# Performance work log

Measured on AMD Instinct MI355X. Metric: run time of the kernel, lower is better.

## Reference

```python
import jax, jax.numpy as jnp
import numpy as np

# Structural metadata (constants): 3 node types, 4 edge types, 2 HGT layers.
T, R, L = 3, 4, 2
H_HID, HEADS, OUT = 256, 8, 128
D = H_HID // HEADS  # per-head dim = 32
SRC_T = (0, 1, 1, 1)  # (author->paper, paper->author, paper->paper, paper->venue)
DST_T = (1, 0, 1, 2)
LN_EPS = 1e-5


def _segment_softmax(logits, seg, n):
    # logits: [E, heads]; softmax over edges sharing the same destination node
    m = jax.ops.segment_max(logits, seg, num_segments=n)
    e = jnp.exp(logits - m[seg])
    s = jax.ops.segment_sum(e, seg, num_segments=n)
    return e / s[seg]


def setup_inputs() -> dict:
    key = jax.random.key(0)
    ks = iter(jax.random.split(key, 64))
    N, E, FIN = 20000, 60000, 128

    def nrm(shape, scale):
        return jax.random.normal(next(ks), shape, jnp.float32) * scale

    return dict(
        x=jax.random.normal(next(ks), (T, N, FIN), jnp.float32),
        edge_index=jax.random.randint(next(ks), (R, 2, E), 0, N),
        Win=nrm((T, FIN, H_HID), 0.05),
        b_in=jnp.zeros((T, H_HID), jnp.float32),
        Wk=nrm((L, T, H_HID, H_HID), 0.05), bk=jnp.zeros((L, T, H_HID), jnp.float32),
        Wq=nrm((L, T, H_HID, H_HID), 0.05), bq=jnp.zeros((L, T, H_HID), jnp.float32),
        Wv=nrm((L, T, H_HID, H_HID), 0.05), bv=jnp.zeros((L, T, H_HID), jnp.float32),
        Wa=nrm((L, T, H_HID, H_HID), 0.05), ba=jnp.zeros((L, T, H_HID), jnp.float32),
        skip=jnp.ones((L, T), jnp.float32),
        a_rel=nrm((L, R, HEADS, D, D), 0.1),
        m_rel=nrm((L, R, HEADS, D, D), 0.1),
        p_rel=jnp.ones((L, R, HEADS), jnp.float32),
        ln_g=jnp.ones((L, T, H_HID), jnp.float32),
        ln_b=jnp.zeros((L, T, H_HID), jnp.float32),
        Wout=nrm((H_HID, OUT), 0.05),
        bout=jnp.zeros((OUT,), jnp.float32),
    )


def reference(x, edge_index, Win, b_in, Wk, bk, Wq, bq, Wv, bv, Wa, ba,
              skip, a_rel, m_rel, p_rel, ln_g, ln_b, Wout, bout):
    N = x.shape[1]
    inv_sqrt_d = jnp.float32(1.0 / np.sqrt(D))
    # Input projection + ReLU (dropout = identity in eval mode)
    h = jax.nn.relu(jnp.einsum('tnf,tfh->tnh', x, Win) + b_in[:, None, :])

    for l in range(L):
        res = h
        # Per-node-type k/q/v projections, reshaped to heads
        k = (jnp.einsum('tnh,tho->tno', h, Wk[l]) + bk[l][:, None]).reshape(T, N, HEADS, D)
        q = (jnp.einsum('tnh,tho->tno', h, Wq[l]) + bq[l][:, None]).reshape(T, N, HEADS, D)
        v = (jnp.einsum('tnh,tho->tno', h, Wv[l]) + bv[l][:, None]).reshape(T, N, HEADS, D)

        agg = jnp.zeros((T, N, HEADS, D), h.dtype)
        for r in range(R):
            st, dt = SRC_T[r], DST_T[r]
            src, dst = edge_index[r, 0], edge_index[r, 1]
            # Per-edge-type relation transforms on source k/v
            k_r = jnp.einsum('nhd,hde->nhe', k[st], a_rel[l, r])
            v_r = jnp.einsum('nhd,hde->nhe', v[st], m_rel[l, r])
            kj = k_r[src]          # [E, heads, d]
            vj = v_r[src]
            qi = q[dt][dst]
            logits = (qi * kj).sum(-1) * p_rel[l, r] * inv_sqrt_d  # [E, heads]
            alpha = _segment_softmax(logits, dst, N)
            msg = vj * alpha[..., None]
            agg = agg.at[dt].add(jax.ops.segment_sum(msg, dst, num_segments=N))

        # Type-specific output linear after exact GELU, gated skip (in==out dims)
        o = jax.nn.gelu(agg.reshape(T, N, H_HID), approximate=False)
        o = jnp.einsum('tnh,tho->tno', o, Wa[l]) + ba[l][:, None]
        beta = jax.nn.sigmoid(skip[l])[:, None, None]
        h = beta * o + (1.0 - beta) * h

        # Model-level residual + LayerNorm + ReLU (dropout = identity)
        h = h + res
        mu = h.mean(-1, keepdims=True)
        var = ((h - mu) ** 2).mean(-1, keepdims=True)
        h = (h - mu) * jax.lax.rsqrt(var + LN_EPS) * ln_g[l][:, None] + ln_b[l][:, None]
        h = jax.nn.relu(h)

    # Shared output projection; outputs stacked over node types: [T, N, OUT]
    return jnp.einsum('tnh,ho->tno', h, Wout) + bout
```

## Files before the change

### kernel.cpp

```cpp
#include <hip/hip_runtime.h>
#include <math.h>

#define T_ 3
#define R_ 4
#define L_ 2
#define H_ 256
#define HEADS_ 8
#define D_ 32
#define FIN_ 128
#define OUT_ 128

typedef unsigned short bf16_t;
typedef __attribute__((ext_vector_type(8))) short bf16x8;
typedef __attribute__((ext_vector_type(4))) float f32x4;

__device__ __forceinline__ float bf2f(bf16_t h) {
    return __uint_as_float(((unsigned)h) << 16);
}
__device__ __forceinline__ float bflo(unsigned u) {
    return __uint_as_float(u << 16);
}
__device__ __forceinline__ float bfhi(unsigned u) {
    return __uint_as_float(u & 0xffff0000u);
}
__device__ __forceinline__ bf16_t f2bf(float f) {
    unsigned u = __float_as_uint(f);
    u += 0x7FFFu + ((u >> 16) & 1u);
    return (bf16_t)(u >> 16);
}
__device__ __forceinline__ float gelu_exact(float x) {
    return 0.5f * x * (1.0f + erff(x * 0.70710678118654752440f));
}

__global__ void zero_kernel(unsigned* __restrict__ p, long n) {
    long i = (long)blockIdx.x * blockDim.x + threadIdx.x;
    long stride = (long)gridDim.x * blockDim.x;
    for (; i < n; i += stride) p[i] = 0u;
}

__global__ __launch_bounds__(256) void transconv2_kernel(
    const float* __restrict__ in0, bf16_t* __restrict__ out0,
    const float* __restrict__ in1, bf16_t* __restrict__ out1,
    int cnt0, int Rr, int Cc)
{
    __shared__ float Ls[64][65];
    const int tid = threadIdx.x;
    int z = blockIdx.z;
    const float* in;
    bf16_t* out;
    if (z < cnt0) { in = in0; out = out0; }
    else          { in = in1; out = out1; z -= cnt0; }
    const long base = (long)z * Rr * Cc;
    const int r0 = blockIdx.y * 64, c0 = blockIdx.x * 64;
    #pragma unroll
    for (int i = 0; i < 16; ++i) {
        int e = tid + i * 256; int row = e >> 6, col = e & 63;
        Ls[row][col] = in[base + (long)(r0 + row) * Cc + c0 + col];
    }
    __syncthreads();
    #pragma unroll
    for (int i = 0; i < 16; ++i) {
        int e = tid + i * 256; int row = e >> 6, col = e & 63;
        out[base + (long)(c0 + row) * Rr + r0 + col] = f2bf(Ls[col][row]);
    }
}

__global__ __launch_bounds__(256) void transconv_kernel(
    const float* __restrict__ in, bf16_t* __restrict__ out, int Rr, int Cc)
{
    __shared__ float Ls[64][65];
    const int tid = threadIdx.x;
    const long base = (long)blockIdx.z * Rr * Cc;
    const int r0 = blockIdx.y * 64, c0 = blockIdx.x * 64;
    #pragma unroll
    for (int i = 0; i < 16; ++i) {
        int e = tid + i * 256; int row = e >> 6, col = e & 63;
        Ls[row][col] = in[base + (long)(r0 + row) * Cc + c0 + col];
    }
    __syncthreads();
    #pragma unroll
    for (int i = 0; i < 16; ++i) {
        int e = tid + i * 256; int row = e >> 6, col = e & 63;
        out[base + (long)(c0 + row) * Rr + r0 + col] = f2bf(Ls[col][row]);
    }
}

__global__ __launch_bounds__(256) void fuse_wT_kernel(
    const float* __restrict__ Wk, const float* __restrict__ Wv,
    const float* __restrict__ bk, const float* __restrict__ bv,
    const float* __restrict__ a_rel, const float* __restrict__ m_rel,
    bf16_t* __restrict__ WkvT, float* __restrict__ bkv)
{
    const int s = blockIdx.z;
    const int kv = s & 1, r = (s >> 1) & 3, l = s >> 3;
    const int SRCT[4] = {0, 1, 1, 1};
    const int st = SRCT[r];
    const float* W = (kv ? Wv : Wk) + ((long)l * T_ + st) * H_ * H_;
    const float* A = (kv ? m_rel : a_rel) + ((long)l * R_ + r) * HEADS_ * D_ * D_;
    const int hh = blockIdx.y, kt = blockIdx.x;
    __shared__ float As[32][33];
    __shared__ float Ws[64][33];
    const int tid = threadIdx.x;
    {
        int d = tid >> 3, e4 = (tid & 7) * 4;
        float4 v = *(const float4*)(A + (hh * D_ + d) * D_ + e4);
        As[d][e4] = v.x; As[d][e4 + 1] = v.y; As[d][e4 + 2] = v.z; As[d][e4 + 3] = v.w;
    }
    #pragma unroll
    for (int p = 0; p < 2; ++p) {
        int idx = p * 256 + tid;
        int row = idx >> 3, c4 = (idx & 7) * 4;
        float4 v = *(const float4*)(W + (long)(kt * 64 + row) * H_ + hh * 32 + c4);
        Ws[row][c4] = v.x; Ws[row][c4 + 1] = v.y; Ws[row][c4 + 2] = v.z; Ws[row][c4 + 3] = v.w;
    }
    __syncthreads();
    const int kl = tid & 63, eb = tid >> 6;
    #pragma unroll
    for (int ii = 0; ii < 8; ++ii) {
        int e = eb * 8 + ii;
        float acc = 0.f;
        #pragma unroll
        for (int d = 0; d < 32; ++d)
            acc += As[d][e] * Ws[kl][d];
        int col = hh * 32 + e;
        int pos = (col >> 2) * 8 + kv * 4 + (col & 3);
        long rowIdx = (long)(s >> 1) * 512 + pos;
        WkvT[rowIdx * H_ + kt * 64 + kl] = f2bf(acc);
    }
    if (blockIdx.x == 0 && blockIdx.y == 0) {
        const float* b = (kv ? bv : bk) + ((long)l * T_ + st) * H_;
        const int bh = tid >> 5, be = tid & 31;
        float acc = 0.f;
        #pragma unroll
        for (int d = 0; d < D_; ++d)
            acc += b[bh * D_ + d] * A[(bh * D_ + d) * D_ + be];
        int pos = (tid >> 2) * 8 + kv * 4 + (tid & 3);
        bkv[(long)(s >> 1) * 512 + pos] = acc;
    }
}

__global__ void hist_kernel(const int* __restrict__ ei, int* __restrict__ indeg,
                            int Nn, int E)
{
    int idx = blockIdx.x * 256 + threadIdx.x;
    if (idx >= R_ * E) return;
    int r = idx / E, e = idx - r * E;
    int d = ei[(size_t)r * 2 * E + E + e];
    atomicAdd(indeg + (size_t)r * Nn + d, 1);
}

__global__ __launch_bounds__(256) void csr_part_kernel(
    const int* __restrict__ indeg, int* __restrict__ partials, int Nn, int nch)
{
    const int r = blockIdx.y, c = blockIdx.x, tid = threadIdx.x;
    const int lane = tid & 63, wave = tid >> 6;
    int idx = c * 256 + tid;
    int v = (idx < Nn) ? indeg[(size_t)r * Nn + idx] : 0;
    #pragma unroll
    for (int off = 1; off < 64; off <<= 1) v += __shfl_xor(v, off);
    __shared__ int wsum[4];
    if (lane == 0) wsum[wave] = v;
    __syncthreads();
    if (tid == 0) partials[r * nch + c] = wsum[0] + wsum[1] + wsum[2] + wsum[3];
}

__global__ __launch_bounds__(256) void csr_scanpart_kernel(
    int* __restrict__ partials, int nch)
{
    const int r = blockIdx.x, tid = threadIdx.x;
    __shared__ int sh[256];
    int v = (tid < nch) ? partials[r * nch + tid] : 0;
    sh[tid] = v;
    __syncthreads();
    for (int off = 1; off < 256; off <<= 1) {
        int u = (tid >= off) ? sh[tid - off] : 0;
        __syncthreads();
        sh[tid] += u;
        __syncthreads();
    }
    if (tid < nch) partials[r * nch + tid] = sh[tid] - v;
}

__global__ __launch_bounds__(256) void csr_write_kernel(
    const int* __restrict__ indeg, const int* __restrict__ partials,
    int* __restrict__ offs, int* __restrict__ cursor, int Nn, int nch)
{
    const int r = blockIdx.y, c = blockIdx.x, tid = threadIdx.x;
    int idx = c * 256 + tid;
    int v = (idx < Nn) ? indeg[(size_t)r * Nn + idx] : 0;
    __shared__ int sh[256];
    sh[tid] = v;
    __syncthreads();
    for (int off = 1; off < 256; off <<= 1) {
        int u = (tid >= off) ? sh[tid - off] : 0;
        __syncthreads();
        sh[tid] += u;
        __syncthreads();
    }
    int incl = sh[tid];
    int base = partials[r * nch + c];
    if (idx < Nn) {
        int excl = base + incl - v;
        offs[(size_t)r * (Nn + 1) + idx] = excl;
        cursor[(size_t)r * Nn + idx] = excl;
        if (idx == Nn - 1) offs[(size_t)r * (Nn + 1) + Nn] = base + incl;
    }
}

__global__ void scatter_kernel(const int* __restrict__ ei, int* __restrict__ cursor,
                               int* __restrict__ esrc, int Nn, int E)
{
    int idx = blockIdx.x * 256 + threadIdx.x;
    if (idx >= R_ * E) return;
    int r = idx / E, e = idx - r * E;
    int s = ei[(size_t)r * 2 * E + e];
    int d = ei[(size_t)r * 2 * E + E + e];
    int pos = atomicAdd(cursor + (size_t)r * Nn + d, 1);
    esrc[(size_t)r * E + pos] = s * 512;
}

#define STEP(rr, vld, prX, mX, sX, x0, x1, x2, x3)                          \
    {                                                                        \
        float dt_ = q0 * bflo(rr.x) + q1 * bfhi(rr.x)                        \
                  + q2 * bflo(rr.y) + q3 * bfhi(rr.y);                       \
        dt_ += __shfl_xor(dt_, 1);                                           \
        dt_ += __shfl_xor(dt_, 2);                                           \
        dt_ += __shfl_xor(dt_, 4);                                           \
        float lg = (vld) ? dt_ * prX : -1e30f;                               \
        if (__any(lg - mX > 8.f)) {                                          \
            float mn = fmaxf(mX, lg);                                        \
            float fac = __expf(mX - mn);                                     \
            float p = __expf(lg - mn);                                       \
            p = (vld) ? p : 0.f;                                             \
            sX = sX * fac + p;                                               \
            x0 = x0 * fac + p * bflo(rr.z);                                  \
            x1 = x1 * fac + p * bfhi(rr.z);                                  \
            x2 = x2 * fac + p * bflo(rr.w);                                  \
            x3 = x3 * fac + p * bfhi(rr.w);                                  \
            mX = mn;                                                         \
        } else {                                                             \
            float p = __expf(lg - mX);                                       \
            p = (vld) ? p : 0.f;                                             \
            sX += p;                                                         \
            x0 += p * bflo(rr.z);                                            \
            x1 += p * bfhi(rr.z);                                            \
            x2 += p * bflo(rr.w);                                            \
            x3 += p * bfhi(rr.w);                                            \
        }                                                                    \
    }

__global__ __launch_bounds__(256) void agg_all_kernel(
    const int* __restrict__ offs, const int* __restrict__ esrc,
    bf16_t* __restrict__ qbuf, const bf16_t* __restrict__ KV,
    const float* __restrict__ p_l, float scale, int Nn, int E)
{
    static const int NRELg[3] = {2, 1, 1};
    static const int R0g[3]  = {0, 1, 3};
    static const int R1g[3]  = {2, 0, 0};
    static const int DTg[3]  = {1, 0, 2};
    const int grp = blockIdx.y;
    const int wave = threadIdx.x >> 6, lane = threadIdx.x & 63;
    const int d = blockIdx.x * 4 + wave;
    if (d >= Nn) return;
    const int head = lane >> 3;
    const int dt = DTg[grp];
    const bool separate = (NRELg[grp] == 2);

    bf16_t* qrow = qbuf + ((size_t)dt * Nn + d) * H_;
    uint2 qu = ((const uint2*)qrow)[lane];
    float q0 = bflo(qu.x), q1 = bfhi(qu.x), q2 = bflo(qu.y), q3 = bfhi(qu.y);

    const int rA = R0g[grp];
    const int* esA = esrc + (size_t)rA * E;
    const bf16_t* kvA = KV + (size_t)rA * Nn * 512;
    float prA = p_l[rA * HEADS_ + head] * scale;
    int curA = offs[(size_t)rA * (Nn + 1) + d];
    int endA = offs[(size_t)rA * (Nn + 1) + d + 1];

    const int* esB; const bf16_t* kvB; float prB;
    int curB, endB;
    if (separate) {
        const int rB = R1g[grp];
        esB = esrc + (size_t)rB * E;
        kvB = KV + (size_t)rB * Nn * 512;
        prB = p_l[rB * HEADS_ + head] * scale;
        curB = offs[(size_t)rB * (Nn + 1) + d];
        endB = offs[(size_t)rB * (Nn + 1) + d + 1];
    } else {
        int mid = curA + ((endA - curA + 1) >> 1);
        esB = esA; kvB = kvA; prB = prA;
        curB = mid; endB = endA;
        endA = mid;
    }
    const int safeA = (endA > 0) ? endA - 1 : 0;
    const int safeB = (endB > 0) ? endB - 1 : 0;
    const int loff = lane * 8;

    float mA = -INFINITY, sA = 0.f, aA0 = 0.f, aA1 = 0.f, aA2 = 0.f, aA3 = 0.f;
    float mB = -INFINITY, sB = 0.f, aB0 = 0.f, aB1 = 0.f, aB2 = 0.f, aB3 = 0.f;

    while (curA < endA || curB < endB) {
        bool vA0 = curA < endA, vA1 = curA + 1 < endA;
        bool vB0 = curB < endB, vB1 = curB + 1 < endB;
        uint4 rA0, rA1, rB0, rB1;
        if (vA0) {
            int i0 = esA[curA];
            int i1 = esA[min(curA + 1, safeA)];
            rA0 = *(const uint4*)(kvA + i0 + loff);
            rA1 = *(const uint4*)(kvA + i1 + loff);
        }
        if (vB0) {
            int i0 = esB[curB];
            int i1 = esB[min(curB + 1, safeB)];
            rB0 = *(const uint4*)(kvB + i0 + loff);
            rB1 = *(const uint4*)(kvB + i1 + loff);
        }
        if (vA0) {
            STEP(rA0, true, prA, mA, sA, aA0, aA1, aA2, aA3)
            STEP(rA1, vA1, prA, mA, sA, aA0, aA1, aA2, aA3)
            curA += 2;
        }
        if (vB0) {
            STEP(rB0, true, prB, mB, sB, aB0, aB1, aB2, aB3)
            STEP(rB1, vB1, prB, mB, sB, aB0, aB1, aB2, aB3)
            curB += 2;
        }
    }

    float t0, t1, t2, t3;
    if (separate) {
        float iA = (sA > 0.f) ? 1.f / sA : 0.f;
        float iB = (sB > 0.f) ? 1.f / sB : 0.f;
        t0 = aA0 * iA + aB0 * iB;
        t1 = aA1 * iA + aB1 * iB;
        t2 = aA2 * iA + aB2 * iB;
        t3 = aA3 * iA + aB3 * iB;
    } else {
        if (sB > 0.f) {
            float mm = fmaxf(mA, mB);
            float fx = (sA > 0.f) ? __expf(mA - mm) : 0.f;
            float fy = __expf(mB - mm);
            sA = sA * fx + sB * fy;
            aA0 = aA0 * fx + aB0 * fy;
            aA1 = aA1 * fx + aB1 * fy;
            aA2 = aA2 * fx + aB2 * fy;
            aA3 = aA3 * fx + aB3 * fy;
        }
        float iA = (sA > 0.f) ? 1.f / sA : 0.f;
        t0 = aA0 * iA; t1 = aA1 * iA; t2 = aA2 * iA; t3 = aA3 * iA;
    }
    ushort4 ou;
    ou.x = f2bf(gelu_exact(t0));
    ou.y = f2bf(gelu_exact(t1));
    ou.z = f2bf(gelu_exact(t2));
    ou.w = f2bf(gelu_exact(t3));
    ((ushort4*)qrow)[lane] = ou;
}

#define ASTR 40
#define ESTR 72

template<typename TA, typename TC, int ACT_C>
__global__ __launch_bounds__(256) void mfma_gemm(
    const TA* __restrict__ A, const TA* __restrict__ A2, int zsplit,
    const bf16_t* __restrict__ BT,
    const float* __restrict__ bias, TC* __restrict__ C,
    int M, int K, int Nc,
    long strideA, long strideB, long strideBias, long strideC)
{
    const int gX = gridDim.x, gY = gridDim.y, gZ = gridDim.z;
    const int nwg = gX * gY * gZ;
    int flat = blockIdx.x + gX * (blockIdx.y + gY * blockIdx.z);
    const int qch = nwg >> 3, rch = nwg & 7;
    int xcd = flat & 7, cidx = flat >> 3;
    int swz = (xcd < rch ? xcd * (qch + 1) : rch * (qch + 1) + (xcd - rch) * qch) + cidx;
    const int by = swz / (gX * gZ);
    int rem = swz - by * (gX * gZ);
    const int bz = rem / gX;
    const int bx = rem - bz * gX;

    const TA* Ab = (bz < zsplit) ? (A + (long)bz * strideA) : A2;
    const bf16_t* Bb = BT + (long)bz * strideB;
    const float* biasb = bias + (long)bz * strideBias;
    TC* Cb = C + (long)bz * strideC;

    __shared__ bf16_t As[128 * ASTR];
    __shared__ bf16_t Bs[128 * ASTR];
    __shared__ bf16_t Es[4 * 16 * ESTR];
    const int tid = threadIdx.x;
    const int lane = tid & 63, wave = tid >> 6;
    const int wr = wave >> 1, wc = wave & 1;
    const int bm = by * 128, bn = bx * 128;
    const int r16 = lane & 15, g = lane >> 4;
    f32x4 acc[4][4] = {};

    for (int k0 = 0; k0 < K; k0 += 32) {
        #pragma unroll
        for (int p = 0; p < 2; ++p) {
            int idx = p * 256 + tid;
            int row = idx >> 2, seg = idx & 3;
            int grow = bm + row;
            bf16x8 av = {};
            if (grow < M) {
                if constexpr (sizeof(TA) == 2) {
                    av = *(const bf16x8*)(Ab + (long)grow * K + k0 + seg * 8);
                } else {
                    const float* sp = (const float*)Ab + (long)grow * K + k0 + seg * 8;
                    float4 f0 = *(const float4*)sp, f1 = *(const float4*)(sp + 4);
                    av[0] = (short)f2bf(f0.x); av[1] = (short)f2bf(f0.y);
                    av[2] = (short)f2bf(f0.z); av[3] = (short)f2bf(f0.w);
                    av[4] = (short)f2bf(f1.x); av[5] = (short)f2bf(f1.y);
                    av[6] = (short)f2bf(f1.z); av[7] = (short)f2bf(f1.w);
                }
            }
            *(bf16x8*)(As + row * ASTR + seg * 8) = av;
            bf16x8 bv = *(const bf16x8*)(Bb + (long)(bn + row) * K + k0 + seg * 8);
            *(bf16x8*)(Bs + row * ASTR + seg * 8) = bv;
        }
        __syncthreads();
        bf16x8 af[4], bfr[4];
        #pragma unroll
        for (int m = 0; m < 4; ++m)
            af[m] = *(const bf16x8*)(As + (wr * 64 + m * 16 + r16) * ASTR + g * 8);
        #pragma unroll
        for (int n = 0; n < 4; ++n)
            bfr[n] = *(const bf16x8*)(Bs + (wc * 64 + n * 16 + r16) * ASTR + g * 8);
        #pragma unroll
        for (int m = 0; m < 4; ++m)
            #pragma unroll
            for (int n = 0; n < 4; ++n)
                acc[m][n] = __builtin_amdgcn_mfma_f32_16x16x32_bf16(af[m], bfr[n], acc[m][n], 0, 0, 0);
        __syncthreads();
    }

    float bb[4];
    #pragma unroll
    for (int n = 0; n < 4; ++n)
        bb[n] = biasb[bn + wc * 64 + n * 16 + r16];

    if constexpr (sizeof(TC) == 2) {
        bf16_t* st = Es + wave * (16 * ESTR);
        #pragma unroll
        for (int m = 0; m < 4; ++m) {
            int rowbase = bm + wr * 64 + m * 16;
            #pragma unroll
            for (int n = 0; n < 4; ++n) {
                #pragma unroll
                for (int j = 0; j < 4; ++j) {
                    float vv = acc[m][n][j] + bb[n];
                    if (ACT_C) vv = fmaxf(vv, 0.f);
                    st[(g * 4 + j) * ESTR + n * 16 + r16] = f2bf(vv);
                }
            }
            #pragma unroll
            for (int p = 0; p < 2; ++p) {
                int row = p * 8 + (lane >> 3);
                int col0 = (lane & 7) * 8;
                int grow = rowbase + row;
                bf16x8 val = *(const bf16x8*)(st + row * ESTR + col0);
                if (grow < M)
                    *(bf16x8*)(Cb + (long)grow * Nc + bn + wc * 64 + col0) = val;
            }
        }
    } else {
        #pragma unroll
        for (int n = 0; n < 4; ++n) {
            int col = bn + wc * 64 + n * 16 + r16;
            #pragma unroll
            for (int m = 0; m < 4; ++m) {
                int rowbase = bm + wr * 64 + m * 16 + g * 4;
                #pragma unroll
                for (int j = 0; j < 4; ++j) {
                    int row = rowbase + j;
                    if (row < M) {
                        float vv = acc[m][n][j] + bb[n];
                        if (ACT_C) vv = fmaxf(vv, 0.f);
                        Cb[(long)row * Nc + col] = vv;
                    }
                }
            }
        }
    }
}

__global__ __launch_bounds__(512) void gemm_ln_kernel(
    const bf16_t* __restrict__ A,
    const bf16_t* __restrict__ BT,
    const float* __restrict__ bias,
    bf16_t* __restrict__ h,
    const float* __restrict__ skip_l,
    const float* __restrict__ ln_g,
    const float* __restrict__ ln_b,
    int M)
{
    const int gY = gridDim.y;
    const int nwg = gY * 3;
    int flat = blockIdx.y + gY * blockIdx.z;
    const int qch = nwg >> 3, rch = nwg & 7;
    int xcd = flat & 7, cidx = flat >> 3;
    int swz = (xcd < rch ? xcd * (qch + 1) : rch * (qch + 1) + (xcd - rch) * qch) + cidx;
    const int by = swz / 3;
    const int bz = swz - by * 3;

    const bf16_t* Ab = A + (long)bz * M * H_;
    const bf16_t* Bb = BT + (long)bz * H_ * H_;
    const float* biasb = bias + bz * H_;
    bf16_t* hb = h + (long)bz * M * H_;
    const float* lgp = ln_g + bz * H_;
    const float* lbp = ln_b + bz * H_;

    __shared__ bf16_t As[128 * ASTR];
    __shared__ bf16_t Bs[256 * ASTR];
    __shared__ bf16_t Es[8 * 16 * ESTR];
    __shared__ float  sums[128][4][2];

    const int tid = threadIdx.x;
    const int lane = tid & 63, wave = tid >> 6;
    const int wr = wave >> 2, wc = wave & 3;
    const int bm = by * 128;
    const int r16 = lane & 15, g = lane >> 4;
    f32x4 acc[4][4] = {};

    for (int k0 = 0; k0 < H_; k0 += 32) {
        {
            int row = tid >> 2, seg = tid & 3;
            int grow = bm + row;
            bf16x8 av = {};
            if (grow < M) av = *(const bf16x8*)(Ab + (long)grow * H_ + k0 + seg * 8);
            *(bf16x8*)(As + row * ASTR + seg * 8) = av;
        }
        #pragma unroll
        for (int p = 0; p < 2; ++p) {
            int idx = p * 512 + tid;
            int row = idx >> 2, seg = idx & 3;
            bf16x8 bv = *(const bf16x8*)(Bb + (long)row * H_ + k0 + seg * 8);
            *(bf16x8*)(Bs + row * ASTR + seg * 8) = bv;
        }
        __syncthreads();
        bf16x8 af[4], bfr[4];
        #pragma unroll
        for (int m = 0; m < 4; ++m)
            af[m] = *(const bf16x8*)(As + (wr * 64 + m * 16 + r16) * ASTR + g * 8);
        #pragma unroll
        for (int n = 0; n < 4; ++n)
            bfr[n] = *(const bf16x8*)(Bs + (wc * 64 + n * 16 + r16) * ASTR + g * 8);
        #pragma unroll
        for (int m = 0; m < 4; ++m)
            #pragma unroll
            for (int n = 0; n < 4; ++n)
                acc[m][n] = __builtin_amdgcn_mfma_f32_16x16x32_bf16(af[m], bfr[n], acc[m][n], 0, 0, 0);
        __syncthreads();
    }

    const float beta = 1.f / (1.f + __expf(-skip_l[bz]));
    const float cb = 2.f - beta;
    const int colb = wc * 64;
    float bb[4], lng[4], lnb[4];
    #pragma unroll
    for (int n = 0; n < 4; ++n) {
        int col = colb + n * 16 + r16;
        bb[n] = biasb[col]; lng[n] = lgp[col]; lnb[n] = lbp[col];
    }

    bf16_t* st = Es + wave * (16 * ESTR);
    #pragma unroll
    for (int m = 0; m < 4; ++m) {
        #pragma unroll
        for (int p = 0; p < 2; ++p) {
            int row = p * 8 + (lane >> 3);
            int col0 = (lane & 7) * 8;
            int grow = bm + wr * 64 + m * 16 + row;
            bf16x8 hv = {};
            if (grow < M) hv = *(const bf16x8*)(hb + (long)grow * H_ + colb + col0);
            *(bf16x8*)(st + row * ESTR + col0) = hv;
        }
        #pragma unroll
        for (int j = 0; j < 4; ++j) {
            int lrow = wr * 64 + m * 16 + g * 4 + j;
            float s1 = 0.f, s2 = 0.f;
            #pragma unroll
            for (int n = 0; n < 4; ++n) {
                float o = acc[m][n][j] + bb[n];
                float hv = bf2f(st[(g * 4 + j) * ESTR + n * 16 + r16]);
                float u = beta * o + cb * hv;
                acc[m][n][j] = u;
                s1 += u; s2 += u * u;
            }
            s1 += __shfl_xor(s1, 1); s2 += __shfl_xor(s2, 1);
            s1 += __shfl_xor(s1, 2); s2 += __shfl_xor(s2, 2);
            s1 += __shfl_xor(s1, 4); s2 += __shfl_xor(s2, 4);
            s1 += __shfl_xor(s1, 8); s2 += __shfl_xor(s2, 8);
            if (r16 == 0) { sums[lrow][wc][0] = s1; sums[lrow][wc][1] = s2; }
        }
    }
    __syncthreads();

    #pragma unroll
    for (int m = 0; m < 4; ++m) {
        #pragma unroll
        for (int j = 0; j < 4; ++j) {
            int lrow = wr * 64 + m * 16 + g * 4 + j;
            float S1 = sums[lrow][0][0] + sums[lrow][1][0] + sums[lrow][2][0] + sums[lrow][3][0];
            float S2 = sums[lrow][0][1] + sums[lrow][1][1] + sums[lrow][2][1] + sums[lrow][3][1];
            float mu = S1 * (1.f / H_);
            float var = S2 * (1.f / H_) - mu * mu;
            float inv = rsqrtf(var + 1e-5f);
            #pragma unroll
            for (int n = 0; n < 4; ++n) {
                float r = fmaxf((acc[m][n][j] - mu) * inv * lng[n] + lnb[n], 0.f);
                st[(g * 4 + j) * ESTR + n * 16 + r16] = f2bf(r);
            }
        }
        #pragma unroll
        for (int p = 0; p < 2; ++p) {
            int row = p * 8 + (lane >> 3);
            int col0 = (lane & 7) * 8;
            int grow = bm + wr * 64 + m * 16 + row;
            bf16x8 val = *(const bf16x8*)(st + row * ESTR + col0);
            if (grow < M)
                *(bf16x8*)(hb + (long)grow * H_ + colb + col0) = val;
        }
    }
}

extern "C" void kernel_launch(void* const* d_in, const int* in_sizes, int n_in,
                              void* d_out, int out_size, void* d_ws, size_t ws_size,
                              hipStream_t stream)
{
    const float* x     = (const float*)d_in[0];
    const int*   ei    = (const int*)  d_in[1];
    const float* Win   = (const float*)d_in[2];
    const float* b_in  = (const float*)d_in[3];
    const float* Wk    = (const float*)d_in[4];
    const float* bk    = (const float*)d_in[5];
    const float* Wq    = (const float*)d_in[6];
    const float* bq    = (const float*)d_in[7];
    const float* Wv    = (const float*)d_in[8];
    const float* bv    = (const float*)d_in[9];
    const float* Wa    = (const float*)d_in[10];
    const float* ba    = (const float*)d_in[11];
    const float* skip  = (const float*)d_in[12];
    const float* a_rel = (const float*)d_in[13];
    const float* m_rel = (const float*)d_in[14];
    const float* p_rel = (const float*)d_in[15];
    const float* ln_g  = (const float*)d_in[16];
    const float* ln_b  = (const float*)d_in[17];
    const float* Wout  = (const float*)d_in[18];
    const float* bout  = (const float*)d_in[19];
    float* out = (float*)d_out;

    const int N = in_sizes[0] / (T_ * FIN_);
    const int E = in_sizes[1] / (R_ * 2);
    const size_t NH = (size_t)N * H_;
    const int nch = (N + 255) / 256;
    const int ZBIG = 1 << 20;

    char* wp = (char*)d_ws;
    auto alloc = [&](size_t bytes) {
        void* r = wp;
        wp += (bytes + 255) & ~(size_t)255;
        return r;
    };
    bf16_t* h     = (bf16_t*)alloc(T_ * NH * 2);
    bf16_t* qbuf  = (bf16_t*)alloc(T_ * NH * 2);
    bf16_t* KV    = (bf16_t*)alloc((size_t)R_ * N * 512 * 2);
    int*    indeg = (int*)   alloc((size_t)R_ * N * 4);
    int*    offs  = (int*)   alloc((size_t)R_ * (N + 1) * 4);
    int*    cursor= (int*)   alloc((size_t)R_ * N * 4);
    int*    esrc  = (int*)   alloc((size_t)R_ * E * 4);
    int*    parts = (int*)   alloc((size_t)R_ * 256 * 4);
    bf16_t* WqT   = (bf16_t*)alloc((size_t)L_ * T_ * H_ * H_ * 2);
    bf16_t* WaT   = (bf16_t*)alloc((size_t)L_ * T_ * H_ * H_ * 2);
    bf16_t* WinT  = (bf16_t*)alloc((size_t)T_ * FIN_ * H_ * 2);
    bf16_t* WoutT = (bf16_t*)alloc((size_t)H_ * OUT_ * 2);
    bf16_t* WkvT  = (bf16_t*)alloc((size_t)L_ * R_ * 512 * H_ * 2);
    float*  bkv   = (float*) alloc((size_t)L_ * R_ * 512 * 4);

    if ((size_t)(wp - (char*)d_ws) > ws_size) return;

    const float scale = 0.17677669529663688f;
    dim3 blk(256);
    auto gM = [](long M) { return (int)((M + 127) / 128); };

    transconv2_kernel<<<dim3(4, 4, 2 * L_ * T_), blk, 0, stream>>>(
        Wq, WqT, Wa, WaT, L_ * T_, H_, H_);
    transconv_kernel<<<dim3(4, 2, T_), blk, 0, stream>>>(Win, WinT, FIN_, H_);
    transconv_kernel<<<dim3(2, 4, 1),  blk, 0, stream>>>(Wout, WoutT, H_, OUT_);
    fuse_wT_kernel<<<dim3(4, 8, 16), blk, 0, stream>>>(
        Wk, Wv, bk, bv, a_rel, m_rel, WkvT, bkv);

    zero_kernel<<<256, blk, 0, stream>>>((unsigned*)indeg, (long)R_ * N);
    hist_kernel<<<(R_ * E + 255) / 256, blk, 0, stream>>>(ei, indeg, N, E);
    csr_part_kernel<<<dim3(nch, R_), blk, 0, stream>>>(indeg, parts, N, nch);
    csr_scanpart_kernel<<<R_, blk, 0, stream>>>(parts, nch);
    csr_write_kernel<<<dim3(nch, R_), blk, 0, stream>>>(indeg, parts, offs, cursor, N, nch);
    scatter_kernel<<<(R_ * E + 255) / 256, blk, 0, stream>>>(ei, cursor, esrc, N, E);

    mfma_gemm<float, bf16_t, 1><<<dim3(H_ / 128, gM(N), T_), blk, 0, stream>>>(
        x, x, ZBIG, WinT, b_in, h, N, FIN_, H_,
        (long)N * FIN_, (long)FIN_ * H_, H_, (long)NH);

    for (int l = 0; l < L_; ++l) {
        const long lw = (long)l * R_;
        mfma_gemm<bf16_t, bf16_t, 0><<<dim3(512 / 128, gM(N), 4), blk, 0, stream>>>(
            h, h + NH, 1, WkvT + lw * 512 * H_, bkv + lw * 512, KV,
            N, H_, 512, 0L, 512L * H_, 512L, (long)N * 512);
        mfma_gemm<bf16_t, bf16_t, 0><<<dim3(H_ / 128, gM(N), 3), blk, 0, stream>>>(
            h, h, ZBIG, WqT + (size_t)l * T_ * H_ * H_, bq + (size_t)l * T_ * H_, qbuf,
            N, H_, H_, (long)NH, (long)H_ * H_, (long)H_, (long)NH);
        agg_all_kernel<<<dim3((N + 3) / 4, 3), blk, 0, stream>>>(
            offs, esrc, qbuf, KV, p_rel + (size_t)l * R_ * HEADS_, scale, N, E);
        gemm_ln_kernel<<<dim3(1, gM(N), 3), dim3(512), 0, stream>>>(
            qbuf, WaT + (size_t)l * T_ * H_ * H_, ba + (size_t)l * T_ * H_,
            h, skip + l * T_, ln_g + (size_t)l * T_ * H_, ln_b + (size_t)l * T_ * H_, N);
    }

    mfma_gemm<bf16_t, float, 0><<<dim3(OUT_ / 128, gM((long)T_ * N), 1), blk, 0, stream>>>(
        h, h, ZBIG, WoutT, bout, out, T_ * N, H_, OUT_, 0L, 0L, 0L, 0L);
}
```

Measured before the change: 401.6 us.

## Merge setup, CSR build and KV/Q GEMMs into fewer launches; use exp2 softmax

Three transpose-convert kernels become one, and the six CSR-building kernels become a single cooperative kernel that separates its phases with grid-wide syncs. The per-layer KV and Q projection GEMMs become one kvq_gemm launch with an XCD-swizzled tile map. The online softmax now uses exp2f with the log2(e) factor folded into the scale. The goal is to cut launch count and per-launch overhead. The cooperative grid syncs and the idle out-of-range blocks in the merged GEMM add some cost of their own.

Result: slower. 651.9 us (+62.3%).

```diff
diff --git a/kernel.cpp b/kernel.cpp
--- a/kernel.cpp
+++ b/kernel.cpp
@@ -1,5 +1,8 @@
 #include <hip/hip_runtime.h>
+#include <hip/hip_cooperative_groups.h>
 #include <math.h>
+
+namespace cg = cooperative_groups;
 
 #define T_ 3
 #define R_ 4
@@ -32,46 +35,23 @@
     return 0.5f * x * (1.0f + erff(x * 0.70710678118654752440f));
 }
 
-__global__ void zero_kernel(unsigned* __restrict__ p, long n) {
-    long i = (long)blockIdx.x * blockDim.x + threadIdx.x;
-    long stride = (long)gridDim.x * blockDim.x;
-    for (; i < n; i += stride) p[i] = 0u;
-}
-
-__global__ __launch_bounds__(256) void transconv2_kernel(
-    const float* __restrict__ in0, bf16_t* __restrict__ out0,
-    const float* __restrict__ in1, bf16_t* __restrict__ out1,
-    int cnt0, int Rr, int Cc)
+__global__ __launch_bounds__(256) void transconv_all_kernel(
+    const float* __restrict__ Wq, const float* __restrict__ Wa,
+    const float* __restrict__ Win, const float* __restrict__ Wout,
+    bf16_t* __restrict__ WqT, bf16_t* __restrict__ WaT,
+    bf16_t* __restrict__ WinT, bf16_t* __restrict__ WoutT)
 {
     __shared__ float Ls[64][65];
+    int z = blockIdx.z;
+    const float* in; bf16_t* out; int Rr, Cc;
+    if (z < 6)       { in = Wq;   out = WqT;   Rr = 256; Cc = 256; }
+    else if (z < 12) { in = Wa;   out = WaT;   Rr = 256; Cc = 256; z -= 6; }
+    else if (z < 15) { in = Win;  out = WinT;  Rr = 128; Cc = 256; z -= 12; }
+    else             { in = Wout; out = WoutT; Rr = 256; Cc = 128; z = 0; }
+    const int r0 = blockIdx.y * 64, c0 = blockIdx.x * 64;
+    if (r0 >= Rr || c0 >= Cc) return;
     const int tid = threadIdx.x;
-    int z = blockIdx.z;
-    const float* in;
-    bf16_t* out;
-    if (z < cnt0) { in = in0; out = out0; }
-    else          { in = in1; out = out1; z -= cnt0; }
     const long base = (long)z * Rr * Cc;
-    const int r0 = blockIdx.y * 64, c0 = blockIdx.x * 64;
-    #pragma unroll
-    for (int i = 0; i < 16; ++i) {
-        int e = tid + i * 256; int row = e >> 6, col = e & 63;
-        Ls[row][col] = in[base + (long)(r0 + row) * Cc + c0 + col];
-    }
-    __syncthreads();
-    #pragma unroll
-    for (int i = 0; i < 16; ++i) {
-        int e = tid + i * 256; int row = e >> 6, col = e & 63;
-        out[base + (long)(c0 + row) * Rr + r0 + col] = f2bf(Ls[col][row]);
-    }
-}
-
-__global__ __launch_bounds__(256) void transconv_kernel(
-    const float* __restrict__ in, bf16_t* __restrict__ out, int Rr, int Cc)
-{
-    __shared__ float Ls[64][65];
-    const int tid = threadIdx.x;
-    const long base = (long)blockIdx.z * Rr * Cc;
-    const int r0 = blockIdx.y * 64, c0 = blockIdx.x * 64;
     #pragma unroll
     for (int i = 0; i < 16; ++i) {
         int e = tid + i * 256; int row = e >> 6, col = e & 63;
@@ -139,84 +119,89 @@
     }
 }
 
-__global__ void hist_kernel(const int* __restrict__ ei, int* __restrict__ indeg,
-                            int Nn, int E)
+__global__ __launch_bounds__(256) void csr_coop_kernel(
+    const int* __restrict__ ei, int* __restrict__ indeg,
+    int* __restrict__ offs, int* __restrict__ cursor,
+    int* __restrict__ esrc, int* __restrict__ parts,
+    int Nn, int E, int nch)
 {
-    int idx = blockIdx.x * 256 + threadIdx.x;
-    if (idx >= R_ * E) return;
-    int r = idx / E, e = idx - r * E;
-    int d = ei[(size_t)r * 2 * E + E + e];
-    atomicAdd(indeg + (size_t)r * Nn + d, 1);
-}
-
-__global__ __launch_bounds__(256) void csr_part_kernel(
-    const int* __restrict__ indeg, int* __restrict__ partials, int Nn, int nch)
-{
-    const int r = blockIdx.y, c = blockIdx.x, tid = threadIdx.x;
-    const int lane = tid & 63, wave = tid >> 6;
-    int idx = c * 256 + tid;
-    int v = (idx < Nn) ? indeg[(size_t)r * Nn + idx] : 0;
-    #pragma unroll
-    for (int off = 1; off < 64; off <<= 1) v += __shfl_xor(v, off);
+    cg::grid_group grid = cg::this_grid();
+    const int tid = threadIdx.x;
+    const long gsz = (long)gridDim.x * 256;
+    const long gt = (long)blockIdx.x * 256 + tid;
+    __shared__ int sh[256];
     __shared__ int wsum[4];
-    if (lane == 0) wsum[wave] = v;
-    __syncthreads();
-    if (tid == 0) partials[r * nch + c] = wsum[0] + wsum[1] + wsum[2] + wsum[3];
-}
-
-__global__ __launch_bounds__(256) void csr_scanpart_kernel(
-    int* __restrict__ partials, int nch)
-{
-    const int r = blockIdx.x, tid = threadIdx.x;
-    __shared__ int sh[256];
-    int v = (tid < nch) ? partials[r * nch + tid] : 0;
-    sh[tid] = v;
-    __syncthreads();
-    for (int off = 1; off < 256; off <<= 1) {
-        int u = (tid >= off) ? sh[tid - off] : 0;
-        __syncthreads();
-        sh[tid] += u;
-        __syncthreads();
-    }
-    if (tid < nch) partials[r * nch + tid] = sh[tid] - v;
-}
-
-__global__ __launch_bounds__(256) void csr_write_kernel(
-    const int* __restrict__ indeg, const int* __restrict__ partials,
-    int* __restrict__ offs, int* __restrict__ cursor, int Nn, int nch)
-{
-    const int r = blockIdx.y, c = blockIdx.x, tid = threadIdx.x;
-    int idx = c * 256 + tid;
-    int v = (idx < Nn) ? indeg[(size_t)r * Nn + idx] : 0;
-    __shared__ int sh[256];
-    sh[tid] = v;
-    __syncthreads();
-    for (int off = 1; off < 256; off <<= 1) {
-        int u = (tid >= off) ? sh[tid - off] : 0;
-        __syncthreads();
-        sh[tid] += u;
-        __syncthreads();
-    }
-    int incl = sh[tid];
-    int base = partials[r * nch + c];
-    if (idx < Nn) {
-        int excl = base + incl - v;
-        offs[(size_t)r * (Nn + 1) + idx] = excl;
-        cursor[(size_t)r * Nn + idx] = excl;
-        if (idx == Nn - 1) offs[(size_t)r * (Nn + 1) + Nn] = base + incl;
-    }
-}
-
-__global__ void scatter_kernel(const int* __restrict__ ei, int* __restrict__ cursor,
-                               int* __restrict__ esrc, int Nn, int E)
-{
-    int idx = blockIdx.x * 256 + threadIdx.x;
-    if (idx >= R_ * E) return;
-    int r = idx / E, e = idx - r * E;
-    int s = ei[(size_t)r * 2 * E + e];
-    int d = ei[(size_t)r * 2 * E + E + e];
-    int pos = atomicAdd(cursor + (size_t)r * Nn + d, 1);
-    esrc[(size_t)r * E + pos] = s * 512;
+
+    for (long i = gt; i < (long)R_ * Nn; i += gsz) indeg[i] = 0;
+    grid.sync();
+
+    for (long i = gt; i < (long)R_ * E; i += gsz) {
+        int r = (int)(i / E), e = (int)(i - (long)r * E);
+        int d = ei[(long)r * 2 * E + E + e];
+        atomicAdd(indeg + (long)r * Nn + d, 1);
+    }
+    grid.sync();
+
+    for (int c = blockIdx.x; c < R_ * nch; c += gridDim.x) {
+        int r = c / nch, ch = c - r * nch;
+        int idx = ch * 256 + tid;
+        int v = (idx < Nn) ? indeg[(long)r * Nn + idx] : 0;
+        int lane = tid & 63, wave = tid >> 6;
+        #pragma unroll
+        for (int off = 1; off < 64; off <<= 1) v += __shfl_xor(v, off);
+        if (lane == 0) wsum[wave] = v;
+        __syncthreads();
+        if (tid == 0) parts[c] = wsum[0] + wsum[1] + wsum[2] + wsum[3];
+        __syncthreads();
+    }
+    grid.sync();
+
+    if (blockIdx.x < R_) {
+        int r = blockIdx.x;
+        int v = (tid < nch) ? parts[r * nch + tid] : 0;
+        sh[tid] = v;
+        __syncthreads();
+        for (int off = 1; off < 256; off <<= 1) {
+            int u = (tid >= off) ? sh[tid - off] : 0;
+            __syncthreads();
+            sh[tid] += u;
+            __syncthreads();
+        }
+        if (tid < nch) parts[r * nch + tid] = sh[tid] - v;
+    }
+    grid.sync();
+
+    for (int c = blockIdx.x; c < R_ * nch; c += gridDim.x) {
+        int r = c / nch, ch = c - r * nch;
+        int idx = ch * 256 + tid;
+        int v = (idx < Nn) ? indeg[(long)r * Nn + idx] : 0;
+        sh[tid] = v;
+        __syncthreads();
+        for (int off = 1; off < 256; off <<= 1) {
+            int u = (tid >= off) ? sh[tid - off] : 0;
+            __syncthreads();
+            sh[tid] += u;
+            __syncthreads();
+        }
+        int incl = sh[tid];
+        int base = parts[c];
+        if (idx < Nn) {
+            int excl = base + incl - v;
+            offs[(long)r * (Nn + 1) + idx] = excl;
+            cursor[(long)r * Nn + idx] = excl;
+            if (idx == Nn - 1) offs[(long)r * (Nn + 1) + Nn] = base + incl;
+        }
+        __syncthreads();
+    }
+    grid.sync();
+
+    for (long i = gt; i < (long)R_ * E; i += gsz) {
+        int r = (int)(i / E), e = (int)(i - (long)r * E);
+        int s = ei[(long)r * 2 * E + e];
+        int d = ei[(long)r * 2 * E + E + e];
+        int pos = atomicAdd(cursor + (long)r * Nn + d, 1);
+        esrc[(long)r * E + pos] = s * 512;
+    }
 }
 
 #define STEP(rr, vld, prX, mX, sX, x0, x1, x2, x3)                          \
@@ -227,10 +212,10 @@
         dt_ += __shfl_xor(dt_, 2);                                           \
         dt_ += __shfl_xor(dt_, 4);                                           \
         float lg = (vld) ? dt_ * prX : -1e30f;                               \
-        if (__any(lg - mX > 8.f)) {                                          \
+        if (__any(lg - mX > 11.5415603f)) {                                  \
             float mn = fmaxf(mX, lg);                                        \
-            float fac = __expf(mX - mn);                                     \
-            float p = __expf(lg - mn);                                       \
+            float fac = exp2f(mX - mn);                                      \
+            float p = exp2f(lg - mn);                                        \
             p = (vld) ? p : 0.f;                                             \
             sX = sX * fac + p;                                               \
             x0 = x0 * fac + p * bflo(rr.z);                                  \
@@ -239,7 +224,7 @@
             x3 = x3 * fac + p * bfhi(rr.w);                                  \
             mX = mn;                                                         \
         } else {                                                             \
-            float p = __expf(lg - mX);                                       \
+            float p = exp2f(lg - mX);                                        \
             p = (vld) ? p : 0.f;                                             \
             sX += p;                                                         \
             x0 += p * bflo(rr.z);                                            \
@@ -252,7 +237,7 @@
 __global__ __launch_bounds__(256) void agg_all_kernel(
     const int* __restrict__ offs, const int* __restrict__ esrc,
     bf16_t* __restrict__ qbuf, const bf16_t* __restrict__ KV,
-    const float* __restrict__ p_l, float scale, int Nn, int E)
+    const float* __restrict__ p_l, float scale2, int Nn, int E)
 {
     static const int NRELg[3] = {2, 1, 1};
     static const int R0g[3]  = {0, 1, 3};
@@ -273,7 +258,7 @@
     const int rA = R0g[grp];
     const int* esA = esrc + (size_t)rA * E;
     const bf16_t* kvA = KV + (size_t)rA * Nn * 512;
-    float prA = p_l[rA * HEADS_ + head] * scale;
+    float prA = p_l[rA * HEADS_ + head] * scale2;
     int curA = offs[(size_t)rA * (Nn + 1) + d];
     int endA = offs[(size_t)rA * (Nn + 1) + d + 1];
 
@@ -283,7 +268,7 @@
         const int rB = R1g[grp];
         esB = esrc + (size_t)rB * E;
         kvB = KV + (size_t)rB * Nn * 512;
-        prB = p_l[rB * HEADS_ + head] * scale;
+        prB = p_l[rB * HEADS_ + head] * scale2;
         curB = offs[(size_t)rB * (Nn + 1) + d];
         endB = offs[(size_t)rB * (Nn + 1) + d + 1];
     } else {
@@ -338,8 +323,8 @@
     } else {
         if (sB > 0.f) {
             float mm = fmaxf(mA, mB);
-            float fx = (sA > 0.f) ? __expf(mA - mm) : 0.f;
-            float fy = __expf(mB - mm);
+            float fx = (sA > 0.f) ? exp2f(mA - mm) : 0.f;
+            float fy = exp2f(mB - mm);
             sA = sA * fx + sB * fy;
             aA0 = aA0 * fx + aB0 * fy;
             aA1 = aA1 * fx + aB1 * fy;
@@ -483,15 +468,114 @@
     }
 }
 
+__global__ __launch_bounds__(256) void kvq_gemm(
+    const bf16_t* __restrict__ h, const bf16_t* __restrict__ WkvT_l,
+    const float* __restrict__ bkv_l, const bf16_t* __restrict__ WqT_l,
+    const float* __restrict__ bq_l, bf16_t* __restrict__ KV,
+    bf16_t* __restrict__ qbuf, int M, long NH)
+{
+    const int gX = gridDim.x, gY = gridDim.y, gZ = gridDim.z;
+    const int nwg = gX * gY * gZ;
+    int flat = blockIdx.x + gX * (blockIdx.y + gY * blockIdx.z);
+    const int qch = nwg >> 3, rch = nwg & 7;
+    int xcd = flat & 7, cidx = flat >> 3;
+    int swz = (xcd < rch ? xcd * (qch + 1) : rch * (qch + 1) + (xcd - rch) * qch) + cidx;
+    const int by = swz / (gX * gZ);
+    int rem = swz - by * (gX * gZ);
+    const int bz = rem / gX;
+    const int bx = rem - bz * gX;
+
+    int Nc;
+    const bf16_t* Ab; const bf16_t* Bb; const float* biasb; bf16_t* Cb;
+    if (bz < 4) {
+        const int SRCT[4] = {0, 1, 1, 1};
+        Ab = h + (long)SRCT[bz] * NH;
+        Bb = WkvT_l + (long)bz * 512 * H_;
+        biasb = bkv_l + bz * 512;
+        Cb = KV + (long)bz * M * 512;
+        Nc = 512;
+    } else {
+        if (bx >= 2) return;
+        int t = bz - 4;
+        Ab = h + (long)t * NH;
+        Bb = WqT_l + (long)t * H_ * H_;
+        biasb = bq_l + t * H_;
+        Cb = qbuf + (long)t * NH;
+        Nc = 256;
+    }
+
+    __shared__ bf16_t As[128 * ASTR];
+    __shared__ bf16_t Bs[128 * ASTR];
+    __shared__ bf16_t Es[4 * 16 * ESTR];
+    const int tid = threadIdx.x;
+    const int lane = tid & 63, wave = tid >> 6;
+    const int wr = wave >> 1, wc = wave & 1;
+    const int bm = by * 128, bn = bx * 128;
+    const int r16 = lane & 15, g = lane >> 4;
+    f32x4 acc[4][4] = {};
+
+    for (int k0 = 0; k0 < H_; k0 += 32) {
+        #pragma unroll
+        for (int p = 0; p < 2; ++p) {
+            int idx = p * 256 + tid;
+            int row = idx >> 2, seg = idx & 3;
+            int grow = bm + row;
+            bf16x8 av = {};
+            if (grow < M) av = *(const bf16x8*)(Ab + (long)grow * H_ + k0 + seg * 8);
+            *(bf16x8*)(As + row * ASTR + seg * 8) = av;
+            bf16x8 bv = *(const bf16x8*)(Bb + (long)(bn + row) * H_ + k0 + seg * 8);
+            *(bf16x8*)(Bs + row * ASTR + seg * 8) = bv;
+        }
+        __syncthreads();
+        bf16x8 af[4], bfr[4];
+        #pragma unroll
+        for (int m = 0; m < 4; ++m)
+            af[m] = *(const bf16x8*)(As + (wr * 64 + m * 16 + r16) * ASTR + g * 8);
+        #pragma unroll
+        for (int n = 0; n < 4; ++n)
+            bfr[n] = *(const bf16x8*)(Bs + (wc * 64 + n * 16 + r16) * ASTR + g * 8);
+        #pragma unroll
+        for (int m = 0; m < 4; ++m)
+            #pragma unroll
+            for (int n = 0; n < 4; ++n)
+                acc[m][n] = __builtin_amdgcn_mfma_f32_16x16x32_bf16(af[m], bfr[n], acc[m][n], 0, 0, 0);
+        __syncthreads();
+    }
+
+    float bb[4];
+    #pragma unroll
+    for (int n = 0; n < 4; ++n)
+        bb[n] = biasb[bn + wc * 64 + n * 16 + r16];
+
+    bf16_t* st = Es + wave * (16 * ESTR);
+    #pragma unroll
+    for (int m = 0; m < 4; ++m) {
+        int rowbase = bm + wr * 64 + m * 16;
+        #pragma unroll
+        for (int n = 0; n < 4; ++n) {
+            #pragma unroll
+            for (int j = 0; j < 4; ++j) {
+                float vv = acc[m][n][j] + bb[n];
+                st[(g * 4 + j) * ESTR + n * 16 + r16] = f2bf(vv);
+            }
+        }
+        #pragma unroll
+        for (int p = 0; p < 2; ++p) {
+            int row = p * 8 + (lane >> 3);
+            int col0 = (lane & 7) * 8;
+            int grow = rowbase + row;
+            bf16x8 val = *(const bf16x8*)(st + row * ESTR + col0);
+            if (grow < M)
+                *(bf16x8*)(Cb + (long)grow * Nc + bn + wc * 64 + col0) = val;
+        }
+    }
+}
+
 __global__ __launch_bounds__(512) void gemm_ln_kernel(
-    const bf16_t* __restrict__ A,
-    const bf16_t* __restrict__ BT,
-    const float* __restrict__ bias,
-    bf16_t* __restrict__ h,
-    const float* __restrict__ skip_l,
-    const float* __restrict__ ln_g,
-    const float* __restrict__ ln_b,
-    int M)
+    const bf16_t* __restrict__ A, const bf16_t* __restrict__ BT,
+    const float* __restrict__ bias, bf16_t* __restrict__ h,
+    const float* __restrict__ skip_l, const float* __restrict__ ln_g,
+    const float* __restrict__ ln_b, int M)
 {
     const int gY = gridDim.y;
     const int nwg = gY * 3;
@@ -678,23 +762,21 @@
 
     if ((size_t)(wp - (char*)d_ws) > ws_size) return;
 
-    const float scale = 0.17677669529663688f;
+    const float scale2 = 0.17677669529663688f * 1.4426950408889634f;
     dim3 blk(256);
     auto gM = [](long M) { return (int)((M + 127) / 128); };
 
-    transconv2_kernel<<<dim3(4, 4, 2 * L_ * T_), blk, 0, stream>>>(
-        Wq, WqT, Wa, WaT, L_ * T_, H_, H_);
-    transconv_kernel<<<dim3(4, 2, T_), blk, 0, stream>>>(Win, WinT, FIN_, H_);
-    transconv_kernel<<<dim3(2, 4, 1),  blk, 0, stream>>>(Wout, WoutT, H_, OUT_);
+    transconv_all_kernel<<<dim3(4, 4, 16), blk, 0, stream>>>(
+        Wq, Wa, Win, Wout, WqT, WaT, WinT, WoutT);
     fuse_wT_kernel<<<dim3(4, 8, 16), blk, 0, stream>>>(
         Wk, Wv, bk, bv, a_rel, m_rel, WkvT, bkv);
 
-    zero_kernel<<<256, blk, 0, stream>>>((unsigned*)indeg, (long)R_ * N);
-    hist_kernel<<<(R_ * E + 255) / 256, blk, 0, stream>>>(ei, indeg, N, E);
-    csr_part_kernel<<<dim3(nch, R_), blk, 0, stream>>>(indeg, parts, N, nch);
-    csr_scanpart_kernel<<<R_, blk, 0, stream>>>(parts, nch);
-    csr_write_kernel<<<dim3(nch, R_), blk, 0, stream>>>(indeg, parts, offs, cursor, N, nch);
-    scatter_kernel<<<(R_ * E + 255) / 256, blk, 0, stream>>>(ei, cursor, esrc, N, E);
+    {
+        int nN = N, nE = E, nC = nch;
+        void* args[] = { (void*)&ei, (void*)&indeg, (void*)&offs, (void*)&cursor,
+                         (void*)&esrc, (void*)&parts, (void*)&nN, (void*)&nE, (void*)&nC };
+        hipLaunchCooperativeKernel((void*)csr_coop_kernel, dim3(512), blk, args, 0, stream);
+    }
 
     mfma_gemm<float, bf16_t, 1><<<dim3(H_ / 128, gM(N), T_), blk, 0, stream>>>(
         x, x, ZBIG, WinT, b_in, h, N, FIN_, H_,
@@ -702,14 +784,12 @@
 
     for (int l = 0; l < L_; ++l) {
         const long lw = (long)l * R_;
-        mfma_gemm<bf16_t, bf16_t, 0><<<dim3(512 / 128, gM(N), 4), blk, 0, stream>>>(
-            h, h + NH, 1, WkvT + lw * 512 * H_, bkv + lw * 512, KV,
-            N, H_, 512, 0L, 512L * H_, 512L, (long)N * 512);
-        mfma_gemm<bf16_t, bf16_t, 0><<<dim3(H_ / 128, gM(N), 3), blk, 0, stream>>>(
-            h, h, ZBIG, WqT + (size_t)l * T_ * H_ * H_, bq + (size_t)l * T_ * H_, qbuf,
-            N, H_, H_, (long)NH, (long)H_ * H_, (long)H_, (long)NH);
+        kvq_gemm<<<dim3(4, gM(N), 7), blk, 0, stream>>>(
+            h, WkvT + lw * 512 * H_, bkv + lw * 512,
+            WqT + (size_t)l * T_ * H_ * H_, bq + (size_t)l * T_ * H_,
+            KV, qbuf, N, (long)NH);
         agg_all_kernel<<<dim3((N + 3) / 4, 3), blk, 0, stream>>>(
-            offs, esrc, qbuf, KV, p_rel + (size_t)l * R_ * HEADS_, scale, N, E);
+            offs, esrc, qbuf, KV, p_rel + (size_t)l * R_ * HEADS_, scale2, N, E);
         gemm_ln_kernel<<<dim3(1, gM(N), 3), dim3(512), 0, stream>>>(
             qbuf, WaT + (size_t)l * T_ * H_ * H_, ba + (size_t)l * T_ * H_,
             h, skip + l * T_, ln_g + (size_t)l * T_ * H_, ln_b + (size_t)l * T_ * H_, N);
```
